# Kernel tuning notes

Measured on AMD Instinct MI355X. Metric: run time of the kernel, lower is better.

## Reference

```python
import jax, jax.numpy as jnp
import numpy as np

TPF = 36           # tokens per frame (fixed in source)
K = 4              # context frames
D = 1024           # embed_dim
H = 16             # n_heads
HD = D // H        # head_dim = 64
L = 8              # n_layers
V = 4096           # vocab_size
NA = 2             # n_actions
NL = 8             # n_levels
B = 64             # batch
S = K * (TPF + 1) + TPF   # 184


def _build_mask():
    block_idx = np.zeros(S, dtype=np.int64)
    pos = 0
    for i in range(K):
        block_idx[pos:pos + TPF] = 2 * i
        pos += TPF
        block_idx[pos] = 2 * i + 1
        pos += 1
    block_idx[pos:] = 2 * K
    mask = block_idx[:, None] < block_idx[None, :]
    ctx_end = K * (TPF + 1)
    # causal within the target frame block
    tri = np.triu(np.ones((TPF, TPF), dtype=bool), k=1)
    mask[ctx_end:ctx_end + TPF, ctx_end:ctx_end + TPF] |= tri
    return mask  # (S, S) bool, True = blocked


def _build_rope(theta=10000.0):
    freqs = 1.0 / theta ** (np.arange(0, HD, 2, dtype=np.float32) / HD)  # (HD/2,)
    t = np.arange(S, dtype=np.float32)
    ang = np.outer(t, freqs)  # (S, HD/2)
    return np.cos(ang), np.sin(ang)


def setup_inputs() -> dict:
    key = jax.random.key(0)
    ks = iter(jax.random.split(key, 40))

    def nrm(shape):
        return jax.random.normal(next(ks), shape, jnp.float32) * 0.02

    cos, sin = _build_rope()
    inp = dict(
        frame_tokens=jax.random.randint(next(ks), (B, K + 1, TPF), 0, V),
        actions=jax.random.randint(next(ks), (B, K), 0, NA),
        level_ids=jax.random.randint(next(ks), (B,), 0, NL),
        tok_emb=nrm((V, D)),
        act_emb=nrm((NA, D)),
        lvl_emb=nrm((NL, D)),
        ln1_g=jnp.ones((L, D)), ln1_b=jnp.zeros((L, D)),
        qkv_w=nrm((L, 3 * D, D)), qkv_b=jnp.zeros((L, 3 * D)),
        out_w=nrm((L, D, D)), out_b=jnp.zeros((L, D)),
        ln2_g=jnp.ones((L, D)), ln2_b=jnp.zeros((L, D)),
        mlp_w1=nrm((L, 4 * D, D)), mlp_b1=jnp.zeros((L, 4 * D)),
        mlp_w2=nrm((L, D, 4 * D)), mlp_b2=jnp.zeros((L, D)),
        lnf_g=jnp.ones((D,)), lnf_b=jnp.zeros((D,)),
        head_w=nrm((V, D)),
        death_w=nrm((1, D)), death_b=jnp.zeros((1,)),
        rope_cos=jnp.asarray(cos), rope_sin=jnp.asarray(sin),
        attn_mask=jnp.asarray(_build_mask()),
    )
    return inp


def _ln(x, g, b, eps=1e-5):
    m = x.mean(-1, keepdims=True)
    v = x.var(-1, keepdims=True)
    return (x - m) / jnp.sqrt(v + eps) * g + b


def _rope(x, cos, sin):
    # x: (B,H,T,HD); cos/sin: (T, HD/2)
    d = x.shape[-1] // 2
    x1, x2 = x[..., :d], x[..., d:]
    return jnp.concatenate([x1 * cos - x2 * sin, x1 * sin + x2 * cos], axis=-1)


def reference(frame_tokens, actions, level_ids, tok_emb, act_emb, lvl_emb,
              ln1_g, ln1_b, qkv_w, qkv_b, out_w, out_b, ln2_g, ln2_b,
              mlp_w1, mlp_b1, mlp_w2, mlp_b2, lnf_g, lnf_b,
              head_w, death_w, death_b, rope_cos, rope_sin, attn_mask):
    b = frame_tokens.shape[0]
    # interleave: [frame_i tokens (36), action_i (1)] * K, then target frame (36)
    parts = []
    for i in range(K):
        parts.append(tok_emb[frame_tokens[:, i]])          # (B, 36, D)
        parts.append(act_emb[actions[:, i]][:, None, :])   # (B, 1, D)
    parts.append(tok_emb[frame_tokens[:, K]])
    x = jnp.concatenate(parts, axis=1)                     # (B, S, D)
    x = x + lvl_emb[level_ids][:, None, :]

    scale = HD ** -0.5
    for l in range(L):
        h = _ln(x, ln1_g[l], ln1_b[l])
        qkv = h @ qkv_w[l].T + qkv_b[l]                    # (B, S, 3D)
        qkv = qkv.reshape(b, S, 3, H, HD).transpose(2, 0, 3, 1, 4)
        q, k, v = qkv[0], qkv[1], qkv[2]                   # (B, H, S, HD)
        q = _rope(q, rope_cos, rope_sin)
        k = _rope(k, rope_cos, rope_sin)
        att = jnp.einsum('bhqd,bhkd->bhqk', q, k) * scale
        att = jnp.where(attn_mask, -jnp.inf, att)
        att = jax.nn.softmax(att, axis=-1)
        h = jnp.einsum('bhqk,bhkd->bhqd', att, v)
        h = h.transpose(0, 2, 1, 3).reshape(b, S, D)
        x = x + (h @ out_w[l].T + out_b[l])
        h2 = _ln(x, ln2_g[l], ln2_b[l])
        h2 = jax.nn.gelu(h2 @ mlp_w1[l].T + mlp_b1[l], approximate=False)
        x = x + (h2 @ mlp_w2[l].T + mlp_b2[l])

    x = _ln(x, lnf_g, lnf_b)
    predict = x[:, S - TPF - 1:S - 1]                      # (B, 36, D)
    logits = predict @ head_w.T                            # (B, 36, V)
    death_logit = x[:, -1] @ death_w.T + death_b           # (B, 1)
    return logits, death_logit
```

## Files before the change

### kernel.cpp

```cpp
#include <hip/hip_runtime.h>
#include <math.h>

#define TPF 36
#define KFRM 4
#define DM 1024
#define NH 16
#define HD 64
#define NLAYER 8
#define VOCAB 4096
#define SEQ 184
#define BATCH 64
#define NTOK (BATCH * SEQ)
#define CTXEND 148

typedef unsigned short u16;
typedef unsigned int u32;
typedef __bf16 bf16x8 __attribute__((ext_vector_type(8)));
typedef float f32x4 __attribute__((ext_vector_type(4)));

struct alignas(8) U16x4 { u16 x, y, z, w; };
struct alignas(16) U16x8 { u16 v[8]; };

__device__ inline u16 f2b(float f) {
  u32 u = __float_as_uint(f);
  u += 0x7FFFu + ((u >> 16) & 1u);
  return (u16)(u >> 16);
}
__device__ inline float b2f(u16 h) { return __uint_as_float(((u32)h) << 16); }

__global__ __launch_bounds__(256) void conv_bf16(const float4* __restrict__ in,
                                                 U16x4* __restrict__ out, int n4) {
  int i = blockIdx.x * 256 + threadIdx.x;
  if (i >= n4) return;
  float4 v = in[i];
  U16x4 o;
  o.x = f2b(v.x); o.y = f2b(v.y); o.z = f2b(v.z); o.w = f2b(v.w);
  out[i] = o;
}

#define CN1 (3072 * 1024 / 4)
#define CN2 (1024 * 1024 / 4)
#define CN3 (4096 * 1024 / 4)
__global__ __launch_bounds__(256) void conv_layer(
    const float4* __restrict__ s1, U16x4* __restrict__ d1,
    const float4* __restrict__ s2, U16x4* __restrict__ d2,
    const float4* __restrict__ s3, U16x4* __restrict__ d3,
    const float4* __restrict__ s4, U16x4* __restrict__ d4) {
  int j = blockIdx.x * 256 + threadIdx.x;
  const float4* s; U16x4* d;
  if (j < CN1) { s = s1; d = d1; }
  else if ((j -= CN1) < CN2) { s = s2; d = d2; }
  else if ((j -= CN2) < CN3) { s = s3; d = d3; }
  else { j -= CN3; s = s4; d = d4; }
  float4 v = s[j];
  U16x4 o;
  o.x = f2b(v.x); o.y = f2b(v.y); o.z = f2b(v.z); o.w = f2b(v.w);
  d[j] = o;
}

__global__ __launch_bounds__(256) void embed_kernel(
    const int* __restrict__ ft, const int* __restrict__ act, const int* __restrict__ lvl,
    const float* __restrict__ tok_emb, const float* __restrict__ act_emb,
    const float* __restrict__ lvl_emb, float* __restrict__ x) {
  int row = blockIdx.x;
  int b = row / SEQ, s = row % SEQ;
  const float* src;
  if (s < CTXEND) {
    int i = s / 37, r = s % 37;
    if (r < 36) src = tok_emb + (size_t)ft[(b * 5 + i) * TPF + r] * DM;
    else        src = act_emb + (size_t)act[b * KFRM + i] * DM;
  } else {
    src = tok_emb + (size_t)ft[(b * 5 + 4) * TPF + (s - CTXEND)] * DM;
  }
  const float* le = lvl_emb + (size_t)lvl[b] * DM;
  float* dst = x + (size_t)row * DM;
  for (int d = threadIdx.x; d < DM; d += 256) dst[d] = src[d] + le[d];
}

__global__ __launch_bounds__(256) void ln_rows(const float* __restrict__ x,
    const float* __restrict__ g, const float* __restrict__ bb,
    u16* __restrict__ out, int nrows) {
  int wid = blockIdx.x * 4 + (threadIdx.x >> 6);
  if (wid >= nrows) return;
  int lane = threadIdx.x & 63;
  const float* row = x + (size_t)wid * DM;
  float s = 0.f, ss = 0.f;
  float v[16];
#pragma unroll
  for (int i = 0; i < 16; i++) {
    v[i] = row[i * 64 + lane];
    s += v[i]; ss += v[i] * v[i];
  }
#pragma unroll
  for (int m = 32; m; m >>= 1) { s += __shfl_xor(s, m, 64); ss += __shfl_xor(ss, m, 64); }
  float mean = s * (1.f / DM);
  float var = ss * (1.f / DM) - mean * mean;
  float rstd = rsqrtf(var + 1e-5f);
  u16* dst = out + (size_t)wid * DM;
#pragma unroll
  for (int i = 0; i < 16; i++) {
    int d = i * 64 + lane;
    dst[d] = f2b((v[i] - mean) * rstd * g[d] + bb[d]);
  }
}

__global__ __launch_bounds__(256) void lnf_kernel(const float* __restrict__ x,
    const float* __restrict__ g, const float* __restrict__ bb,
    u16* __restrict__ pred, float* __restrict__ r183) {
  int wid = blockIdx.x * 4 + (threadIdx.x >> 6);
  if (wid >= BATCH * 37) return;
  int lane = threadIdx.x & 63;
  int b = wid / 37, si = wid % 37, s = 147 + si;
  const float* row = x + ((size_t)b * SEQ + s) * DM;
  float sum = 0.f, ss = 0.f;
  float v[16];
#pragma unroll
  for (int i = 0; i < 16; i++) {
    v[i] = row[i * 64 + lane];
    sum += v[i]; ss += v[i] * v[i];
  }
#pragma unroll
  for (int m = 32; m; m >>= 1) { sum += __shfl_xor(sum, m, 64); ss += __shfl_xor(ss, m, 64); }
  float mean = sum * (1.f / DM);
  float var = ss * (1.f / DM) - mean * mean;
  float rstd = rsqrtf(var + 1e-5f);
  if (s < 183) {
    u16* dst = pred + ((size_t)b * 36 + si) * DM;
#pragma unroll
    for (int i = 0; i < 16; i++) {
      int d = i * 64 + lane;
      dst[d] = f2b((v[i] - mean) * rstd * g[d] + bb[d]);
    }
  } else {
    float* dst = r183 + (size_t)b * DM;
#pragma unroll
    for (int i = 0; i < 16; i++) {
      int d = i * 64 + lane;
      dst[d] = (v[i] - mean) * rstd * g[d] + bb[d];
    }
  }
}

__device__ inline void gld_lds16(const void* g, void* l) {
  __builtin_amdgcn_global_load_lds((const __attribute__((address_space(1))) void*)g,
                                   (__attribute__((address_space(3))) void*)l, 16, 0, 0);
}


template <int BM, int BN, int MODE>
__global__ __launch_bounds__((BM == 256) ? 512 : 256, 2) void gemm_t(
    const u16* __restrict__ A, const u16* __restrict__ W,
    const float* __restrict__ bias, float* __restrict__ Cf, u16* __restrict__ Cb,
    int M, int Kdim) {
  constexpr int WAVES = (BM == 256) ? 8 : 4;
  constexpr int HW = WAVES / 2;
  constexpr int MI = BM / 32;
  __shared__ alignas(16) char As[2][BM * 128];
  __shared__ alignas(16) char Bs[2][BN * 128];
  const int tid = threadIdx.x;
  const int wave = tid >> 6, lane = tid & 63;
  const int wm = wave / HW, wn = wave % HW;
  const int lr = lane & 15, g = lane >> 4;

  const int nbx = gridDim.x;
  int nwg = gridDim.x * gridDim.y;
  int id = blockIdx.y * gridDim.x + blockIdx.x;
  int id2 = (id & 7) * (nwg >> 3) + (id >> 3);
  const int row0 = (id2 / nbx) * BM, col0 = (id2 % nbx) * BN;

  const size_t krow = (size_t)Kdim * 2;
  const char* Abase = (const char*)A + (size_t)row0 * krow;
  const char* Wbase = (const char*)W + (size_t)col0 * krow;

  auto stage = [&](int t, int buf) {
    const char* Ab = Abase + (size_t)t * 128;
    const char* Wb = Wbase + (size_t)t * 128;
#pragma unroll
    for (int c = 0; c < 4; c++) {
      int ob = wave * 4096 + c * 1024;
      int o = ob + lane * 16;
      int os = o ^ (((o >> 7) & 7) << 4);
      gld_lds16(Ab + (size_t)(os >> 7) * krow + (os & 127), &As[buf][ob]);
      gld_lds16(Wb + (size_t)(os >> 7) * krow + (os & 127), &Bs[buf][ob]);
    }
  };

  const int NT = Kdim >> 6;
  f32x4 acc[MI][4] = {};

  stage(0, 0);
  __syncthreads();

#pragma unroll 1
  for (int t = 0; t < NT; t++) {
    int p = t & 1;
    if (t + 1 < NT) stage(t + 1, p ^ 1);
#pragma unroll
    for (int kk = 0; kk < 2; kk++) {
      bf16x8 af[MI], bfj[4];
#pragma unroll
      for (int i = 0; i < MI; i++) {
        int r = wm * (BM / 2) + i * 16 + lr;
        int o = r * 128 + kk * 64 + g * 16;
        af[i] = *(const bf16x8*)(As[p] + (o ^ ((r & 7) << 4)));
      }
#pragma unroll
      for (int j = 0; j < 4; j++) {
        int r = wn * 64 + j * 16 + lr;
        int o = r * 128 + kk * 64 + g * 16;
        bfj[j] = *(const bf16x8*)(Bs[p] + (o ^ ((r & 7) << 4)));
      }
#pragma unroll
      for (int i = 0; i < MI; i++)
#pragma unroll
        for (int j = 0; j < 4; j++)
          acc[i][j] = __builtin_amdgcn_mfma_f32_16x16x32_bf16(af[i], bfj[j], acc[i][j], 0, 0, 0);
    }
    __syncthreads();
  }

  float bj[4];
  if (MODE != 3) {
#pragma unroll
    for (int j = 0; j < 4; j++) bj[j] = bias[col0 + wn * 64 + j * 16 + lr];
  }
#pragma unroll
  for (int i = 0; i < MI; i++) {
#pragma unroll
    for (int j = 0; j < 4; j++) {
#pragma unroll
      for (int r = 0; r < 4; r++) {
        int grow = row0 + wm * (BM / 2) + i * 16 + g * 4 + r;
        int gcol = col0 + wn * 64 + j * 16 + lr;
        float v = acc[i][j][r];
        size_t idx = (size_t)grow * M + gcol;
        if (MODE == 0) { v += bj[j]; Cb[idx] = f2b(v); }
        else if (MODE == 1) { v += bj[j]; Cf[idx] += v; }
        else if (MODE == 2) {
          v += bj[j];
          float z = 1.5957692f * (v + 0.044715f * v * v * v);
          v = v / (1.f + __expf(-z));
          Cb[idx] = f2b(v);
        } else {
          Cf[idx] = v;
        }
      }
    }
  }
}

#define SP 192
#define KST 72
#define VST 200
#define PST 200

__device__ inline int block_of(int s) {
  return (s < CTXEND) ? (2 * (s / 37) + ((s % 37) == 36)) : 8;
}

__global__ __launch_bounds__(256) void attn_mfma(const u16* __restrict__ qkv,
    u16* __restrict__ outb, const float* __restrict__ rc, const float* __restrict__ rs) {
  __shared__ alignas(16) u16 Ks[SP][KST];
  __shared__ alignas(16) u16 Vt[HD][VST];
  __shared__ alignas(16) u16 Ps[4][16][PST];
  const int b = blockIdx.x >> 4, h = blockIdx.x & 15;
  const int tid = threadIdx.x, wave = tid >> 6, lane = tid & 63;
  const int lr = lane & 15, g = lane >> 4, g4 = g * 4;
  const u16* base = qkv + (size_t)b * SEQ * 3072 + h * HD;

  for (int idx = tid; idx < SP * 32; idx += 256) {
    int s = idx >> 5, d = idx & 31;
    if (s < SEQ) {
      const u16* kr = base + (size_t)s * 3072 + 1024;
      float x1 = b2f(kr[d]), x2 = b2f(kr[d + 32]);
      float c = rc[s * 32 + d], sn = rs[s * 32 + d];
      Ks[s][d] = f2b(x1 * c - x2 * sn);
      Ks[s][d + 32] = f2b(x1 * sn + x2 * c);
    } else {
      Ks[s][d] = 0;
      Ks[s][d + 32] = 0;
    }
  }
  for (int idx = tid; idx < SP * HD; idx += 256) {
    int k = idx >> 6, d = idx & 63;
    Vt[d][k] = (k < SEQ) ? base[(size_t)k * 3072 + 2048 + d] : (u16)0;
  }
  __syncthreads();

#pragma unroll 1
  for (int t = 0; t < 3; t++) {
    const int q0 = (wave + 4 * t) * 16;
    const int q_lane = q0 + lr;
    const int qc = (q_lane < SEQ) ? q_lane : (SEQ - 1);

    U16x8 raw0 = *(const U16x8*)(base + (size_t)qc * 3072 + g * 8);
    U16x8 raw1 = *(const U16x8*)(base + (size_t)qc * 3072 + 32 + g * 8);
    bf16x8 qa0, qa1;
#pragma unroll
    for (int i = 0; i < 8; i++) {
      float x1 = b2f(raw0.v[i]), x2 = b2f(raw1.v[i]);
      int di = g * 8 + i;
      float c = rc[qc * 32 + di], sn = rs[qc * 32 + di];
      qa0[i] = (__bf16)(x1 * c - x2 * sn);
      qa1[i] = (__bf16)(x1 * sn + x2 * c);
    }

    f32x4 accs[12];
#pragma unroll
    for (int kt = 0; kt < 12; kt++) accs[kt] = (f32x4){0.f, 0.f, 0.f, 0.f};
#pragma unroll
    for (int kt = 0; kt < 12; kt++) {
      bf16x8 kb0 = *(const bf16x8*)&Ks[kt * 16 + lr][g * 8];
      bf16x8 kb1 = *(const bf16x8*)&Ks[kt * 16 + lr][32 + g * 8];
      accs[kt] = __builtin_amdgcn_mfma_f32_16x16x32_bf16(qa0, kb0, accs[kt], 0, 0, 0);
      accs[kt] = __builtin_amdgcn_mfma_f32_16x16x32_bf16(qa1, kb1, accs[kt], 0, 0, 0);
    }

    int qb[4];
#pragma unroll
    for (int r = 0; r < 4; r++) qb[r] = block_of(q0 + g4 + r);
    float mr[4] = {-3e38f, -3e38f, -3e38f, -3e38f};
#pragma unroll
    for (int kt = 0; kt < 12; kt++) {
      int k = kt * 16 + lr;
      bool kv = k < SEQ;
      int kb = kv ? block_of(k) : 9;
#pragma unroll
      for (int r = 0; r < 4; r++) {
        int q = q0 + g4 + r;
        bool ok = kv && (kb <= qb[r]) && !(q >= CTXEND && k >= CTXEND && k > q);
        float s = ok ? accs[kt][r] * 0.125f : -3e38f;
        accs[kt][r] = s;
        mr[r] = fmaxf(mr[r], s);
      }
    }
#pragma unroll
    for (int m = 1; m <= 8; m <<= 1)
#pragma unroll
      for (int r = 0; r < 4; r++) mr[r] = fmaxf(mr[r], __shfl_xor(mr[r], m, 64));

    float sr[4] = {0.f, 0.f, 0.f, 0.f};
#pragma unroll
    for (int kt = 0; kt < 12; kt++) {
#pragma unroll
      for (int r = 0; r < 4; r++) {
        float e = (accs[kt][r] > -1e37f) ? __expf(accs[kt][r] - mr[r]) : 0.f;
        Ps[wave][g4 + r][kt * 16 + lr] = f2b(e);
        sr[r] += e;
      }
    }
#pragma unroll
    for (int m = 1; m <= 8; m <<= 1)
#pragma unroll
      for (int r = 0; r < 4; r++) sr[r] += __shfl_xor(sr[r], m, 64);
    float inv[4];
#pragma unroll
    for (int r = 0; r < 4; r++) inv[r] = 1.f / sr[r];

    __builtin_amdgcn_s_waitcnt(0);

    f32x4 acco[4];
#pragma unroll
    for (int dt = 0; dt < 4; dt++) acco[dt] = (f32x4){0.f, 0.f, 0.f, 0.f};
#pragma unroll
    for (int kc = 0; kc < 6; kc++) {
      bf16x8 pa = *(const bf16x8*)&Ps[wave][lr][kc * 32 + g * 8];
#pragma unroll
      for (int dt = 0; dt < 4; dt++) {
        bf16x8 vb = *(const bf16x8*)&Vt[dt * 16 + lr][kc * 32 + g * 8];
        acco[dt] = __builtin_amdgcn_mfma_f32_16x16x32_bf16(pa, vb, acco[dt], 0, 0, 0);
      }
    }

#pragma unroll
    for (int dt = 0; dt < 4; dt++) {
#pragma unroll
      for (int r = 0; r < 4; r++) {
        int q = q0 + g4 + r;
        if (q < SEQ)
          outb[((size_t)b * SEQ + q) * DM + h * HD + dt * 16 + lr] = f2b(acco[dt][r] * inv[r]);
      }
    }
  }
}

__global__ void death_kernel(const float* __restrict__ r183, const float* __restrict__ dw,
                             const float* __restrict__ db, float* __restrict__ out) {
  int b = blockIdx.x, lane = threadIdx.x;
  float a = 0.f;
  for (int d = lane; d < DM; d += 64) a += r183[(size_t)b * DM + d] * dw[d];
#pragma unroll
  for (int m = 32; m; m >>= 1) a += __shfl_xor(a, m, 64);
  if (lane == 0) out[(size_t)BATCH * TPF * VOCAB + b] = a + db[0];
}

extern "C" void kernel_launch(void* const* d_in, const int* in_sizes, int n_in,
                              void* d_out, int out_size, void* d_ws, size_t ws_size,
                              hipStream_t stream) {
  const int* ft = (const int*)d_in[0];
  const int* act = (const int*)d_in[1];
  const int* lvl = (const int*)d_in[2];
  const float* tok_emb = (const float*)d_in[3];
  const float* act_emb = (const float*)d_in[4];
  const float* lvl_emb = (const float*)d_in[5];
  const float* ln1_g = (const float*)d_in[6];
  const float* ln1_b = (const float*)d_in[7];
  const float* qkv_w = (const float*)d_in[8];
  const float* qkv_b = (const float*)d_in[9];
  const float* out_w = (const float*)d_in[10];
  const float* out_b = (const float*)d_in[11];
  const float* ln2_g = (const float*)d_in[12];
  const float* ln2_b = (const float*)d_in[13];
  const float* mlp_w1 = (const float*)d_in[14];
  const float* mlp_b1 = (const float*)d_in[15];
  const float* mlp_w2 = (const float*)d_in[16];
  const float* mlp_b2 = (const float*)d_in[17];
  const float* lnf_g = (const float*)d_in[18];
  const float* lnf_b = (const float*)d_in[19];
  const float* head_w = (const float*)d_in[20];
  const float* death_w = (const float*)d_in[21];
  const float* death_b = (const float*)d_in[22];
  const float* rope_cos = (const float*)d_in[23];
  const float* rope_sin = (const float*)d_in[24];

  char* ws = (char*)d_ws;
  size_t off = 0;
  auto alloc = [&](size_t bytes) {
    void* p = ws + off;
    off += (bytes + 255) & ~(size_t)255;
    return p;
  };
  float* x   = (float*)alloc((size_t)NTOK * DM * 4);
  u16* hb    = (u16*)alloc((size_t)NTOK * DM * 2);
  u16* big   = (u16*)alloc((size_t)NTOK * 4096 * 2);
  u16* wq    = (u16*)alloc((size_t)3072 * 1024 * 2);
  u16* wo    = (u16*)alloc((size_t)1024 * 1024 * 2);
  u16* w1    = (u16*)alloc((size_t)4096 * 1024 * 2);
  u16* w2    = (u16*)alloc((size_t)4096 * 1024 * 2);
  u16* pred  = (u16*)alloc((size_t)BATCH * 36 * DM * 2);
  float* r183 = (float*)alloc((size_t)BATCH * DM * 4);

  float* out = (float*)d_out;

  embed_kernel<<<NTOK, 256, 0, stream>>>(ft, act, lvl, tok_emb, act_emb, lvl_emb, x);

  for (int l = 0; l < NLAYER; l++) {
    conv_layer<<<(CN1 + CN2 + 2 * CN3) / 256, 256, 0, stream>>>(
        (const float4*)(qkv_w + (size_t)l * 3072 * 1024), (U16x4*)wq,
        (const float4*)(out_w + (size_t)l * 1024 * 1024), (U16x4*)wo,
        (const float4*)(mlp_w1 + (size_t)l * 4096 * 1024), (U16x4*)w1,
        (const float4*)(mlp_w2 + (size_t)l * 4096 * 1024), (U16x4*)w2);

    ln_rows<<<NTOK / 4, 256, 0, stream>>>(x, ln1_g + l * DM, ln1_b + l * DM, hb, NTOK);
    gemm_t<128, 128, 0><<<dim3(3072 / 128, NTOK / 128), 256, 0, stream>>>(
        hb, wq, qkv_b + (size_t)l * 3072, nullptr, big, 3072, 1024);
    attn_mfma<<<BATCH * NH, 256, 0, stream>>>(big, hb, rope_cos, rope_sin);
    gemm_t<128, 128, 1><<<dim3(1024 / 128, NTOK / 128), 256, 0, stream>>>(
        hb, wo, out_b + (size_t)l * DM, x, nullptr, 1024, 1024);
    ln_rows<<<NTOK / 4, 256, 0, stream>>>(x, ln2_g + l * DM, ln2_b + l * DM, hb, NTOK);
    gemm_t<256, 256, 2><<<dim3(4096 / 256, NTOK / 256), 512, 0, stream>>>(
        hb, w1, mlp_b1 + (size_t)l * 4096, nullptr, big, 4096, 1024);
    gemm_t<128, 128, 1><<<dim3(1024 / 128, NTOK / 128), 256, 0, stream>>>(
        big, w2, mlp_b2 + (size_t)l * DM, x, nullptr, 1024, 4096);
  }

  lnf_kernel<<<BATCH * 37 / 4, 256, 0, stream>>>(x, lnf_g, lnf_b, pred, r183);
  conv_bf16<<<4096 * 1024 / 4 / 256, 256, 0, stream>>>(
      (const float4*)head_w, (U16x4*)w1, 4096 * 1024 / 4);
  gemm_t<128, 128, 3><<<dim3(4096 / 128, BATCH * 36 / 128), 256, 0, stream>>>(
      pred, w1, nullptr, out, nullptr, 4096, 1024);
  death_kernel<<<BATCH, 64, 0, stream>>>(r183, death_w, death_b, out);
}
```

Before: 4.446 ms.

## Replace GEMM with 256x256-tile four-stage pipelined kernel for all projections

Replaces the templated double-buffered GEMM with one 256x256-tile, 512-thread kernel that stages 32-wide K slices into four LDS buffers. Loads are kept three slices ahead, with explicit vmcnt waits and raw barriers in place of __syncthreads, and MFMA priority is raised around the compute block. The aim is to hide global-to-LDS latency and cut barrier stalls. The cost is that the N=1024 GEMMs (out-projection and MLP down) now launch only 184 workgroups, and the 128KB of LDS per block limits each CU to one block, so CU utilisation may drop.

```diff
diff --git a/kernel.cpp b/kernel.cpp
--- a/kernel.cpp
+++ b/kernel.cpp
@@ -146,77 +146,82 @@
                                    (__attribute__((address_space(3))) void*)l, 16, 0, 0);
 }
 
-
-template <int BM, int BN, int MODE>
-__global__ __launch_bounds__((BM == 256) ? 512 : 256, 2) void gemm_t(
+template <int MODE>
+__global__ __launch_bounds__(512, 2) void gemm_p(
     const u16* __restrict__ A, const u16* __restrict__ W,
     const float* __restrict__ bias, float* __restrict__ Cf, u16* __restrict__ Cb,
     int M, int Kdim) {
-  constexpr int WAVES = (BM == 256) ? 8 : 4;
-  constexpr int HW = WAVES / 2;
-  constexpr int MI = BM / 32;
-  __shared__ alignas(16) char As[2][BM * 128];
-  __shared__ alignas(16) char Bs[2][BN * 128];
+  __shared__ alignas(16) char As[4][16384];
+  __shared__ alignas(16) char Bs[4][16384];
   const int tid = threadIdx.x;
   const int wave = tid >> 6, lane = tid & 63;
-  const int wm = wave / HW, wn = wave % HW;
+  const int wm = wave >> 2, wn = wave & 3;
   const int lr = lane & 15, g = lane >> 4;
 
   const int nbx = gridDim.x;
   int nwg = gridDim.x * gridDim.y;
   int id = blockIdx.y * gridDim.x + blockIdx.x;
   int id2 = (id & 7) * (nwg >> 3) + (id >> 3);
-  const int row0 = (id2 / nbx) * BM, col0 = (id2 % nbx) * BN;
+  const int row0 = (id2 / nbx) * 256, col0 = (id2 % nbx) * 256;
 
   const size_t krow = (size_t)Kdim * 2;
   const char* Abase = (const char*)A + (size_t)row0 * krow;
   const char* Wbase = (const char*)W + (size_t)col0 * krow;
 
-  auto stage = [&](int t, int buf) {
-    const char* Ab = Abase + (size_t)t * 128;
-    const char* Wb = Wbase + (size_t)t * 128;
-#pragma unroll
-    for (int c = 0; c < 4; c++) {
-      int ob = wave * 4096 + c * 1024;
+  auto stage = [&](int t, int slot) {
+    const char* Ab = Abase + (size_t)t * 64;
+    const char* Wb = Wbase + (size_t)t * 64;
+#pragma unroll
+    for (int c = 0; c < 2; c++) {
+      int ob = wave * 2048 + c * 1024;
       int o = ob + lane * 16;
-      int os = o ^ (((o >> 7) & 7) << 4);
-      gld_lds16(Ab + (size_t)(os >> 7) * krow + (os & 127), &As[buf][ob]);
-      gld_lds16(Wb + (size_t)(os >> 7) * krow + (os & 127), &Bs[buf][ob]);
+      int os = o ^ (((o >> 7) & 3) << 4);
+      int r = os >> 6, cb = os & 63;
+      gld_lds16(Ab + (size_t)r * krow + cb, &As[slot][ob]);
+      gld_lds16(Wb + (size_t)r * krow + cb, &Bs[slot][ob]);
     }
   };
 
-  const int NT = Kdim >> 6;
-  f32x4 acc[MI][4] = {};
+  const int NT = Kdim >> 5;
+  f32x4 acc[8][4] = {};
 
   stage(0, 0);
-  __syncthreads();
+  stage(1, 1);
+  stage(2, 2);
+  asm volatile("s_waitcnt vmcnt(8)" ::: "memory");
+  asm volatile("s_barrier" ::: "memory");
 
 #pragma unroll 1
   for (int t = 0; t < NT; t++) {
-    int p = t & 1;
-    if (t + 1 < NT) stage(t + 1, p ^ 1);
-#pragma unroll
-    for (int kk = 0; kk < 2; kk++) {
-      bf16x8 af[MI], bfj[4];
-#pragma unroll
-      for (int i = 0; i < MI; i++) {
-        int r = wm * (BM / 2) + i * 16 + lr;
-        int o = r * 128 + kk * 64 + g * 16;
-        af[i] = *(const bf16x8*)(As[p] + (o ^ ((r & 7) << 4)));
-      }
-#pragma unroll
-      for (int j = 0; j < 4; j++) {
-        int r = wn * 64 + j * 16 + lr;
-        int o = r * 128 + kk * 64 + g * 16;
-        bfj[j] = *(const bf16x8*)(Bs[p] + (o ^ ((r & 7) << 4)));
-      }
-#pragma unroll
-      for (int i = 0; i < MI; i++)
-#pragma unroll
-        for (int j = 0; j < 4; j++)
-          acc[i][j] = __builtin_amdgcn_mfma_f32_16x16x32_bf16(af[i], bfj[j], acc[i][j], 0, 0, 0);
-    }
-    __syncthreads();
+    int slot = t & 3;
+    if (t + 3 < NT) stage(t + 3, (t + 3) & 3);
+
+    bf16x8 af[8], bf[4];
+#pragma unroll
+    for (int i = 0; i < 8; i++) {
+      int r = wm * 128 + i * 16 + lr;
+      int o = (r << 6) + (g << 4);
+      af[i] = *(const bf16x8*)(As[slot] + (o ^ (((r >> 1) & 3) << 4)));
+    }
+#pragma unroll
+    for (int j = 0; j < 4; j++) {
+      int r = wn * 64 + j * 16 + lr;
+      int o = (r << 6) + (g << 4);
+      bf[j] = *(const bf16x8*)(Bs[slot] + (o ^ (((r >> 1) & 3) << 4)));
+    }
+    __builtin_amdgcn_s_setprio(1);
+#pragma unroll
+    for (int i = 0; i < 8; i++)
+#pragma unroll
+      for (int j = 0; j < 4; j++)
+        acc[i][j] = __builtin_amdgcn_mfma_f32_16x16x32_bf16(af[i], bf[j], acc[i][j], 0, 0, 0);
+    __builtin_amdgcn_s_setprio(0);
+
+    if (t == NT - 1) break;
+    if (t + 3 < NT)      { asm volatile("s_waitcnt vmcnt(8)" ::: "memory"); }
+    else if (t + 2 < NT) { asm volatile("s_waitcnt vmcnt(4)" ::: "memory"); }
+    else                 { asm volatile("s_waitcnt vmcnt(0)" ::: "memory"); }
+    asm volatile("s_barrier" ::: "memory");
   }
 
   float bj[4];
@@ -225,12 +230,12 @@
     for (int j = 0; j < 4; j++) bj[j] = bias[col0 + wn * 64 + j * 16 + lr];
   }
 #pragma unroll
-  for (int i = 0; i < MI; i++) {
+  for (int i = 0; i < 8; i++) {
 #pragma unroll
     for (int j = 0; j < 4; j++) {
 #pragma unroll
       for (int r = 0; r < 4; r++) {
-        int grow = row0 + wm * (BM / 2) + i * 16 + g * 4 + r;
+        int grow = row0 + wm * 128 + i * 16 + g * 4 + r;
         int gcol = col0 + wn * 64 + j * 16 + lr;
         float v = acc[i][j][r];
         size_t idx = (size_t)grow * M + gcol;
@@ -452,22 +457,22 @@
         (const float4*)(mlp_w2 + (size_t)l * 4096 * 1024), (U16x4*)w2);
 
     ln_rows<<<NTOK / 4, 256, 0, stream>>>(x, ln1_g + l * DM, ln1_b + l * DM, hb, NTOK);
-    gemm_t<128, 128, 0><<<dim3(3072 / 128, NTOK / 128), 256, 0, stream>>>(
+    gemm_p<0><<<dim3(3072 / 256, NTOK / 256), 512, 0, stream>>>(
         hb, wq, qkv_b + (size_t)l * 3072, nullptr, big, 3072, 1024);
     attn_mfma<<<BATCH * NH, 256, 0, stream>>>(big, hb, rope_cos, rope_sin);
-    gemm_t<128, 128, 1><<<dim3(1024 / 128, NTOK / 128), 256, 0, stream>>>(
+    gemm_p<1><<<dim3(1024 / 256, NTOK / 256), 512, 0, stream>>>(
         hb, wo, out_b + (size_t)l * DM, x, nullptr, 1024, 1024);
     ln_rows<<<NTOK / 4, 256, 0, stream>>>(x, ln2_g + l * DM, ln2_b + l * DM, hb, NTOK);
-    gemm_t<256, 256, 2><<<dim3(4096 / 256, NTOK / 256), 512, 0, stream>>>(
+    gemm_p<2><<<dim3(4096 / 256, NTOK / 256), 512, 0, stream>>>(
         hb, w1, mlp_b1 + (size_t)l * 4096, nullptr, big, 4096, 1024);
-    gemm_t<128, 128, 1><<<dim3(1024 / 128, NTOK / 128), 256, 0, stream>>>(
+    gemm_p<1><<<dim3(1024 / 256, NTOK / 256), 512, 0, stream>>>(
         big, w2, mlp_b2 + (size_t)l * DM, x, nullptr, 1024, 4096);
   }
 
   lnf_kernel<<<BATCH * 37 / 4, 256, 0, stream>>>(x, lnf_g, lnf_b, pred, r183);
   conv_bf16<<<4096 * 1024 / 4 / 256, 256, 0, stream>>>(
       (const float4*)head_w, (U16x4*)w1, 4096 * 1024 / 4);
-  gemm_t<128, 128, 3><<<dim3(4096 / 128, BATCH * 36 / 128), 256, 0, stream>>>(
+  gemm_p<3><<<dim3(4096 / 256, BATCH * 36 / 256), 512, 0, stream>>>(
       pred, w1, nullptr, out, nullptr, 4096, 1024);
   death_kernel<<<BATCH, 64, 0, stream>>>(r183, death_w, death_b, out);
 }
```

Result: slower. 5.061 ms (+13.8%).

## Replace GEMM with 256x256 eight-wave kernel using phased loads and raw barriers

Applied to the files above, without the earlier changes.

Replaces the templated GEMM with a single 256x256-tile, 512-thread kernel for every projection. Each K step is split into four quadrant phases. Each phase issues the next tile's quarter-load, then waits with a partial vmcnt and a bare s_barrier, so loads and MFMA work interleave more finely. MFMA priority is raised during compute. The larger tile cuts the block count for the N=1024 and head GEMMs, and the 128KB of LDS per block limits occupancy, which risks underfilling the CUs on the smaller GEMMs.

```diff
diff --git a/kernel.cpp b/kernel.cpp
--- a/kernel.cpp
+++ b/kernel.cpp
@@ -146,103 +146,130 @@
                                    (__attribute__((address_space(3))) void*)l, 16, 0, 0);
 }
 
-
-template <int BM, int BN, int MODE>
-__global__ __launch_bounds__((BM == 256) ? 512 : 256, 2) void gemm_t(
+#define WAITVM(n) asm volatile("s_waitcnt vmcnt(" #n ")" ::: "memory")
+#define BARRIER() asm volatile("s_barrier" ::: "memory")
+
+
+#define GPH_COMPUTE(q)                                                         \
+  {                                                                            \
+    bf16x8 af[2][2], bv[4][2];                                                 \
+    const int ar0 = ((q) & 1) * 128 + (wave & 3) * 32;                         \
+    const int br0 = ((q) >> 1) * 128 + (wave >> 2) * 64;                       \
+    _Pragma("unroll") for (int i = 0; i < 2; i++) {                            \
+      int r = ar0 + i * 16 + lr;                                               \
+      _Pragma("unroll") for (int kk = 0; kk < 2; kk++) {                       \
+        int o = r * 128 + kk * 64 + g * 16;                                    \
+        af[i][kk] = *(const bf16x8*)(Ap + (o ^ ((r & 7) << 4)));               \
+      }                                                                        \
+    }                                                                          \
+    _Pragma("unroll") for (int j = 0; j < 4; j++) {                            \
+      int r = br0 + j * 16 + lr;                                               \
+      _Pragma("unroll") for (int kk = 0; kk < 2; kk++) {                       \
+        int o = r * 128 + kk * 64 + g * 16;                                    \
+        bv[j][kk] = *(const bf16x8*)(Bp + (o ^ ((r & 7) << 4)));               \
+      }                                                                        \
+    }                                                                          \
+    __builtin_amdgcn_s_setprio(1);                                             \
+    _Pragma("unroll") for (int kk = 0; kk < 2; kk++)                           \
+      _Pragma("unroll") for (int i = 0; i < 2; i++)                            \
+        _Pragma("unroll") for (int j = 0; j < 4; j++)                          \
+          acc[q][i][j] = __builtin_amdgcn_mfma_f32_16x16x32_bf16(              \
+              af[i][kk], bv[j][kk], acc[q][i][j], 0, 0, 0);                    \
+    __builtin_amdgcn_s_setprio(0);                                             \
+  }
+
+template <int MODE>
+__global__ __launch_bounds__(512, 2) void gemm8p(
     const u16* __restrict__ A, const u16* __restrict__ W,
     const float* __restrict__ bias, float* __restrict__ Cf, u16* __restrict__ Cb,
     int M, int Kdim) {
-  constexpr int WAVES = (BM == 256) ? 8 : 4;
-  constexpr int HW = WAVES / 2;
-  constexpr int MI = BM / 32;
-  __shared__ alignas(16) char As[2][BM * 128];
-  __shared__ alignas(16) char Bs[2][BN * 128];
+  __shared__ alignas(16) char As[2][32768];
+  __shared__ alignas(16) char Bs[2][32768];
   const int tid = threadIdx.x;
   const int wave = tid >> 6, lane = tid & 63;
-  const int wm = wave / HW, wn = wave % HW;
   const int lr = lane & 15, g = lane >> 4;
 
   const int nbx = gridDim.x;
   int nwg = gridDim.x * gridDim.y;
   int id = blockIdx.y * gridDim.x + blockIdx.x;
   int id2 = (id & 7) * (nwg >> 3) + (id >> 3);
-  const int row0 = (id2 / nbx) * BM, col0 = (id2 % nbx) * BN;
+  const int row0 = (id2 / nbx) * 256, col0 = (id2 % nbx) * 256;
 
   const size_t krow = (size_t)Kdim * 2;
   const char* Abase = (const char*)A + (size_t)row0 * krow;
   const char* Wbase = (const char*)W + (size_t)col0 * krow;
 
-  auto stage = [&](int t, int buf) {
-    const char* Ab = Abase + (size_t)t * 128;
-    const char* Wb = Wbase + (size_t)t * 128;
-#pragma unroll
-    for (int c = 0; c < 4; c++) {
-      int ob = wave * 4096 + c * 1024;
+  auto stage_half = [&](int t, int s, int buf) {
+    const char* src = ((s & 1) ? Wbase : Abase) + (size_t)t * 128;
+    char* lds = (s & 1) ? Bs[buf] : As[buf];
+    int h = s >> 1;
+#pragma unroll
+    for (int c = 0; c < 2; c++) {
+      int ob = h * 16384 + wave * 2048 + c * 1024;
       int o = ob + lane * 16;
       int os = o ^ (((o >> 7) & 7) << 4);
-      gld_lds16(Ab + (size_t)(os >> 7) * krow + (os & 127), &As[buf][ob]);
-      gld_lds16(Wb + (size_t)(os >> 7) * krow + (os & 127), &Bs[buf][ob]);
+      gld_lds16(src + (size_t)(os >> 7) * krow + (os & 127), lds + ob);
     }
   };
 
   const int NT = Kdim >> 6;
-  f32x4 acc[MI][4] = {};
-
-  stage(0, 0);
-  __syncthreads();
+  f32x4 acc[4][2][4] = {};
+
+  stage_half(0, 0, 0);
+  stage_half(0, 1, 0);
+  stage_half(0, 2, 0);
+  stage_half(0, 3, 0);
 
 #pragma unroll 1
-  for (int t = 0; t < NT; t++) {
+  for (int t = 0; t < NT - 1; t++) {
     int p = t & 1;
-    if (t + 1 < NT) stage(t + 1, p ^ 1);
-#pragma unroll
-    for (int kk = 0; kk < 2; kk++) {
-      bf16x8 af[MI], bfj[4];
-#pragma unroll
-      for (int i = 0; i < MI; i++) {
-        int r = wm * (BM / 2) + i * 16 + lr;
-        int o = r * 128 + kk * 64 + g * 16;
-        af[i] = *(const bf16x8*)(As[p] + (o ^ ((r & 7) << 4)));
-      }
+    const char* Ap = As[p];
+    const char* Bp = Bs[p];
+    stage_half(t + 1, 0, p ^ 1); WAITVM(6); BARRIER(); GPH_COMPUTE(0);
+    stage_half(t + 1, 1, p ^ 1); WAITVM(6); BARRIER(); GPH_COMPUTE(1);
+    stage_half(t + 1, 2, p ^ 1); WAITVM(6); BARRIER(); GPH_COMPUTE(2);
+    stage_half(t + 1, 3, p ^ 1); WAITVM(6); BARRIER(); GPH_COMPUTE(3);
+  }
+  {
+    int p = (NT - 1) & 1;
+    const char* Ap = As[p];
+    const char* Bp = Bs[p];
+    WAITVM(4); BARRIER(); GPH_COMPUTE(0);
+    WAITVM(2); BARRIER(); GPH_COMPUTE(1);
+    WAITVM(0); BARRIER(); GPH_COMPUTE(2);
+    BARRIER(); GPH_COMPUTE(3);
+  }
+
+  float bj[2][4];
+  if (MODE != 3) {
+#pragma unroll
+    for (int hb = 0; hb < 2; hb++)
+#pragma unroll
+      for (int j = 0; j < 4; j++)
+        bj[hb][j] = bias[col0 + hb * 128 + (wave >> 2) * 64 + j * 16 + lr];
+  }
+#pragma unroll
+  for (int q = 0; q < 4; q++) {
+#pragma unroll
+    for (int i = 0; i < 2; i++) {
 #pragma unroll
       for (int j = 0; j < 4; j++) {
-        int r = wn * 64 + j * 16 + lr;
-        int o = r * 128 + kk * 64 + g * 16;
-        bfj[j] = *(const bf16x8*)(Bs[p] + (o ^ ((r & 7) << 4)));
-      }
-#pragma unroll
-      for (int i = 0; i < MI; i++)
-#pragma unroll
-        for (int j = 0; j < 4; j++)
-          acc[i][j] = __builtin_amdgcn_mfma_f32_16x16x32_bf16(af[i], bfj[j], acc[i][j], 0, 0, 0);
-    }
-    __syncthreads();
-  }
-
-  float bj[4];
-  if (MODE != 3) {
-#pragma unroll
-    for (int j = 0; j < 4; j++) bj[j] = bias[col0 + wn * 64 + j * 16 + lr];
-  }
-#pragma unroll
-  for (int i = 0; i < MI; i++) {
-#pragma unroll
-    for (int j = 0; j < 4; j++) {
-#pragma unroll
-      for (int r = 0; r < 4; r++) {
-        int grow = row0 + wm * (BM / 2) + i * 16 + g * 4 + r;
-        int gcol = col0 + wn * 64 + j * 16 + lr;
-        float v = acc[i][j][r];
-        size_t idx = (size_t)grow * M + gcol;
-        if (MODE == 0) { v += bj[j]; Cb[idx] = f2b(v); }
-        else if (MODE == 1) { v += bj[j]; Cf[idx] += v; }
-        else if (MODE == 2) {
-          v += bj[j];
-          float z = 1.5957692f * (v + 0.044715f * v * v * v);
-          v = v / (1.f + __expf(-z));
-          Cb[idx] = f2b(v);
-        } else {
-          Cf[idx] = v;
+#pragma unroll
+        for (int r = 0; r < 4; r++) {
+          int grow = row0 + (q & 1) * 128 + (wave & 3) * 32 + i * 16 + g * 4 + r;
+          int gcol = col0 + (q >> 1) * 128 + (wave >> 2) * 64 + j * 16 + lr;
+          float v = acc[q][i][j][r];
+          size_t idx = (size_t)grow * M + gcol;
+          if (MODE == 0) { v += bj[q >> 1][j]; Cb[idx] = f2b(v); }
+          else if (MODE == 1) { v += bj[q >> 1][j]; Cf[idx] += v; }
+          else if (MODE == 2) {
+            v += bj[q >> 1][j];
+            float z = 1.5957692f * (v + 0.044715f * v * v * v);
+            v = v / (1.f + __expf(-z));
+            Cb[idx] = f2b(v);
+          } else {
+            Cf[idx] = v;
+          }
         }
       }
     }
@@ -452,22 +479,22 @@
         (const float4*)(mlp_w2 + (size_t)l * 4096 * 1024), (U16x4*)w2);
 
     ln_rows<<<NTOK / 4, 256, 0, stream>>>(x, ln1_g + l * DM, ln1_b + l * DM, hb, NTOK);
-    gemm_t<128, 128, 0><<<dim3(3072 / 128, NTOK / 128), 256, 0, stream>>>(
+    gemm8p<0><<<dim3(3072 / 256, NTOK / 256), 512, 0, stream>>>(
         hb, wq, qkv_b + (size_t)l * 3072, nullptr, big, 3072, 1024);
     attn_mfma<<<BATCH * NH, 256, 0, stream>>>(big, hb, rope_cos, rope_sin);
-    gemm_t<128, 128, 1><<<dim3(1024 / 128, NTOK / 128), 256, 0, stream>>>(
+    gemm8p<1><<<dim3(1024 / 256, NTOK / 256), 512, 0, stream>>>(
         hb, wo, out_b + (size_t)l * DM, x, nullptr, 1024, 1024);
     ln_rows<<<NTOK / 4, 256, 0, stream>>>(x, ln2_g + l * DM, ln2_b + l * DM, hb, NTOK);
-    gemm_t<256, 256, 2><<<dim3(4096 / 256, NTOK / 256), 512, 0, stream>>>(
+    gemm8p<2><<<dim3(4096 / 256, NTOK / 256), 512, 0, stream>>>(
         hb, w1, mlp_b1 + (size_t)l * 4096, nullptr, big, 4096, 1024);
-    gemm_t<128, 128, 1><<<dim3(1024 / 128, NTOK / 128), 256, 0, stream>>>(
+    gemm8p<1><<<dim3(1024 / 256, NTOK / 256), 512, 0, stream>>>(
         big, w2, mlp_b2 + (size_t)l * DM, x, nullptr, 1024, 4096);
   }
 
   lnf_kernel<<<BATCH * 37 / 4, 256, 0, stream>>>(x, lnf_g, lnf_b, pred, r183);
   conv_bf16<<<4096 * 1024 / 4 / 256, 256, 0, stream>>>(
       (const float4*)head_w, (U16x4*)w1, 4096 * 1024 / 4);
-  gemm_t<128, 128, 3><<<dim3(4096 / 128, BATCH * 36 / 128), 256, 0, stream>>>(
+  gemm8p<3><<<dim3(4096 / 256, BATCH * 36 / 256), 512, 0, stream>>>(
       pred, w1, nullptr, out, nullptr, 4096, 1024);
   death_kernel<<<BATCH, 64, 0, stream>>>(r183, death_w, death_b, out);
 }
```

After: 4.756 ms. 7.0% more time.
